# Optimization experiments

Measured on AMD Instinct MI355X. Metric: run time of the kernel, lower is better.

## Reference

```python
import jax, jax.numpy as jnp
import numpy as np

NUM_HEADS = 12
ROPE_THETA = 100.0

def _rotate_half(x):
    x1 = x[..., ::2]
    x2 = x[..., 1::2]
    return jnp.stack((-x2, x1), axis=-1).reshape(x.shape)

def _apply_rope(x, cos, sin):
    return x * cos + _rotate_half(x) * sin

def _rope_cos_sin(h, w, head_dim, theta):
    quarter = head_dim // 4  # head_dim=64 -> 16 freq bands
    inv_freq = 1.0 / theta ** (jnp.arange(quarter, dtype=jnp.float32) / max(quarter, 1))
    y = jnp.repeat(jnp.arange(h, dtype=jnp.float32), w)   # [h*w]
    xc = jnp.tile(jnp.arange(w, dtype=jnp.float32), h)    # [h*w]
    y_freqs = y[:, None] * inv_freq[None, :]               # [N, quarter]
    x_freqs = xc[:, None] * inv_freq[None, :]
    y_ang = jnp.repeat(y_freqs, 2, axis=-1)                # [N, half]
    x_ang = jnp.repeat(x_freqs, 2, axis=-1)
    ang = jnp.concatenate([y_ang, x_ang], axis=-1)         # [N, head_dim]
    return jnp.cos(ang)[None, None], jnp.sin(ang)[None, None]  # [1,1,N,hd]

def setup_inputs() -> dict:
    key = jax.random.key(0)
    ks = jax.random.split(key, 8)
    B, S, D = 8, 1025, 768
    s = 0.02
    return {
        "x": jax.random.normal(ks[0], (B, S, D), jnp.float32),
        "q_w": jax.random.normal(ks[1], (D, D), jnp.float32) * s,
        "q_b": jax.random.normal(ks[2], (D,), jnp.float32) * s,
        "k_w": jax.random.normal(ks[3], (D, D), jnp.float32) * s,
        "v_w": jax.random.normal(ks[4], (D, D), jnp.float32) * s,
        "v_b": jax.random.normal(ks[5], (D,), jnp.float32) * s,
        "o_w": jax.random.normal(ks[6], (D, D), jnp.float32) * s,
        "o_b": jax.random.normal(ks[7], (D,), jnp.float32) * s,
        "h": 32,
        "w": 32,
        "num_prefix_tokens": 1,
    }

def reference(x, q_w, q_b, k_w, v_w, v_b, o_w, o_b, h, w, num_prefix_tokens):
    B, S, D = x.shape
    H = NUM_HEADS
    hd = D // H
    scale = hd ** -0.5
    p = num_prefix_tokens

    def proj(W, b):
        y = jnp.einsum('bsd,ed->bse', x, W)
        if b is not None:
            y = y + b
        return y.reshape(B, S, H, hd).transpose(0, 2, 1, 3)  # [B,H,S,hd]

    q = proj(q_w, q_b)
    k = proj(k_w, None)
    v = proj(v_w, v_b)

    cos, sin = _rope_cos_sin(h, w, hd, ROPE_THETA)
    q = jnp.concatenate([q[:, :, :p], _apply_rope(q[:, :, p:], cos, sin)], axis=2)
    k = jnp.concatenate([k[:, :, :p], _apply_rope(k[:, :, p:], cos, sin)], axis=2)

    attn = jnp.einsum('bhqd,bhkd->bhqk', q * scale, k)
    attn = jax.nn.softmax(attn, axis=-1)
    out = jnp.einsum('bhqk,bhkd->bhqd', attn, v)
    out = out.transpose(0, 2, 1, 3).reshape(B, S, D)
    return jnp.einsum('bsd,ed->bse', out, o_w) + o_b
```

## Files before the change

### kernel.cpp

```cpp
#include <hip/hip_runtime.h>

typedef unsigned short u16;
typedef unsigned int   u32;
typedef __attribute__((ext_vector_type(4))) short s4;
typedef __attribute__((ext_vector_type(8))) short s8;
typedef __attribute__((ext_vector_type(4))) float f4;
typedef __attribute__((ext_vector_type(16))) float f16v;

#define NB   8
#define SEQ  1025
#define DIM  768
#define NH   12
#define HD   64
#define MPAD 8320
#define MV   8200
#define SQP  1040
#define SKP  1088
#define NQKV 2304
#define BHT  96
#define QSCALE 0.1803368801111204f

__device__ __forceinline__ u16 f2bf(float f) {
  u32 u = __builtin_bit_cast(u32, f);
  u += 0x7fffu + ((u >> 16) & 1u);
  return (u16)(u >> 16);
}
__device__ __forceinline__ float bf2f(u16 h) {
  return __builtin_bit_cast(float, ((u32)h) << 16);
}
__device__ __forceinline__ float exp2f_(float x) {
#if __has_builtin(__builtin_amdgcn_exp2f)
  return __builtin_amdgcn_exp2f(x);
#else
  return exp2f(x);
#endif
}
__device__ __forceinline__ u32 cvtpk(float a, float b) {
  u32 r;
  asm("v_cvt_pk_bf16_f32 %0, %1, %2" : "=v"(r) : "v"(a), "v"(b));
  return r;
}

typedef const __attribute__((address_space(1))) void cas1v;
typedef __attribute__((address_space(3))) void as3v;
__device__ __forceinline__ void gload16(const void* g, void* l) {
  __builtin_amdgcn_global_load_lds((cas1v*)g, (as3v*)l, 16, 0, 0);
}

#define MFMA16(a, b, c) __builtin_amdgcn_mfma_f32_16x16x32_bf16(a, b, c, 0, 0, 0)
#define MFMA32(a, b, c) __builtin_amdgcn_mfma_f32_32x32x16_bf16(a, b, c, 0, 0, 0)

__global__ void conv_x(const float* __restrict__ x, u16* __restrict__ xb) {
  int i = blockIdx.x * 256 + threadIdx.x;
  int e = i * 4;
  int row = e / DIM;
  s4 o;
  if (row < MV) {
    float4 v = *(const float4*)(x + e);
    o[0] = (short)f2bf(v.x); o[1] = (short)f2bf(v.y);
    o[2] = (short)f2bf(v.z); o[3] = (short)f2bf(v.w);
  } else {
    o = (s4){0, 0, 0, 0};
  }
  *(s4*)(xb + e) = o;
}

__global__ void conv_w(const float* __restrict__ qw, const float* __restrict__ kw,
                       const float* __restrict__ vw, const float* __restrict__ ow,
                       const float* __restrict__ qb, const float* __restrict__ vb,
                       u16* __restrict__ wqkv, u16* __restrict__ wo, float* __restrict__ biasq) {
  int i = blockIdx.x * 256 + threadIdx.x;
  wqkv[i]           = f2bf(qw[i]);
  wqkv[i + 589824]  = f2bf(kw[i]);
  wqkv[i + 1179648] = f2bf(vw[i]);
  wo[i]             = f2bf(ow[i]);
  if (i < NQKV) biasq[i] = (i < 768) ? qb[i] : (i < 1536 ? 0.f : vb[i - 1536]);
}

template <int MODE>
__global__ __launch_bounds__(256) void gemm_bt(const u16* __restrict__ A, const u16* __restrict__ Bm,
                                               float* __restrict__ Cf, const float* __restrict__ bias,
                                               u16* __restrict__ Ql, u16* __restrict__ Kl,
                                               u16* __restrict__ Vr,
                                               int N, int K, int Mvalid, int nnt) {
  __shared__ u16 As[2][128 * 32];
  __shared__ u16 Bs[2][128 * 32];
  int tid = threadIdx.x;
  int lane = tid & 63, wave = tid >> 6;
  int g = lane >> 4, c16 = lane & 15;
  int nwg = gridDim.x, orig = blockIdx.x;
  int qd = nwg >> 3, rm = nwg & 7, xcd = orig & 7;
  int wgid = (xcd < rm ? xcd * (qd + 1) : rm * (qd + 1) + (xcd - rm) * qd) + (orig >> 3);
  int m0 = (wgid / nnt) * 128, n0 = (wgid % nnt) * 128;
  int wm = wave >> 1, wn = wave & 1;
  f4 acc[4][4] = {};

  int ldrow = wave * 16 + (lane >> 2);
  int ldk = (lane & 3) * 8;
  const u16* Asrc = A + (size_t)(m0 + ldrow) * K + ldk;
  const u16* Bsrc = Bm + (size_t)(n0 + ldrow) * K + ldk;

  auto stage = [&](int buf, int k0) {
    u16* aw = &As[buf][wave * 512];
    u16* bw = &Bs[buf][wave * 512];
    gload16(Asrc + k0, aw);
    gload16(Asrc + 64 * K + k0, aw + 2048);
    gload16(Bsrc + k0, bw);
    gload16(Bsrc + 64 * K + k0, bw + 2048);
  };

  stage(0, 0);
  __syncthreads();
  int nk = K >> 5;
  for (int t = 0; t < nk; t++) {
    int buf = t & 1;
    if (t + 1 < nk) stage(buf ^ 1, (t + 1) << 5);
    s8 af[4], bf[4];
#pragma unroll
    for (int i = 0; i < 4; i++) {
      af[i] = *(const s8*)(&As[buf][(wm * 64 + i * 16 + c16) * 32 + g * 8]);
      bf[i] = *(const s8*)(&Bs[buf][(wn * 64 + i * 16 + c16) * 32 + g * 8]);
    }
    __builtin_amdgcn_s_setprio(1);
#pragma unroll
    for (int i = 0; i < 4; i++)
#pragma unroll
      for (int j = 0; j < 4; j++)
        acc[i][j] = MFMA16(af[i], bf[j], acc[i][j]);
    __builtin_amdgcn_s_setprio(0);
    __syncthreads();
  }

#pragma unroll
  for (int i = 0; i < 4; i++)
#pragma unroll
    for (int j = 0; j < 4; j++) {
      int n = n0 + wn * 64 + j * 16 + c16;
      float bv = bias[n];
#pragma unroll
      for (int r = 0; r < 4; r++) {
        int m = m0 + wm * 64 + i * 16 + g * 4 + r;
        if (m < Mvalid) {
          float v = acc[i][j][r] + bv;
          if (MODE == 1) {
            Cf[(size_t)m * N + n] = v;
          } else {
            int b = m / 1025, s = m - b * 1025;
            int nh6 = n >> 6, part = nh6 / 12, h = nh6 - part * 12, d = n & 63;
            u16 o = f2bf(v);
            if (part == 0)      Ql[((size_t)((b * NH + h) * SQP + s)) * HD + d] = o;
            else if (part == 1) Kl[((size_t)((b * NH + h) * SKP + s)) * HD + d] = o;
            else                Vr[(size_t)m * DIM + (n - 1536)] = o;
          }
        }
      }
    }
}

__global__ void rope_qk(u16* __restrict__ Ql, u16* __restrict__ Kl) {
  int t = blockIdx.x * 256 + threadIdx.x;
  int j = t & 31;
  int rem = t >> 5;
  int s = rem % SKP;
  int bh = rem / SKP;
  if (bh >= BHT) return;
  size_t qoff = ((size_t)(bh * SQP + s)) * HD + 2 * j;
  size_t koff = ((size_t)(bh * SKP + s)) * HD + 2 * j;
  if (s >= SEQ) {
    *(u32*)(Kl + koff) = 0;
    if (s < SQP) *(u32*)(Ql + qoff) = 0;
    return;
  }
  u32 qp = *(const u32*)(Ql + qoff);
  u32 kp = *(const u32*)(Kl + koff);
  float q0 = bf2f((u16)qp), q1 = bf2f((u16)(qp >> 16));
  float k0 = bf2f((u16)kp), k1 = bf2f((u16)(kp >> 16));
  float cs = 1.f, sn = 0.f;
  if (s > 0) {
    int tok = s - 1;
    int pos = (j < 16) ? (tok >> 5) : (tok & 31);
    int f = j & 15;
    float ang = (float)pos * __expf((float)f * -0.28782313662425572f);
    __sincosf(ang, &sn, &cs);
  }
  float q0r = q0 * cs - q1 * sn, q1r = q1 * cs + q0 * sn;
  float k0r = k0 * cs - k1 * sn, k1r = k1 * cs + k0 * sn;
  *(u32*)(Ql + qoff) = (u32)f2bf(q0r * QSCALE) | ((u32)f2bf(q1r * QSCALE) << 16);
  *(u32*)(Kl + koff) = (u32)f2bf(k0r) | ((u32)f2bf(k1r) << 16);
}

__global__ void v_trans(const u16* __restrict__ Vr, u16* __restrict__ Vt) {
  __shared__ u16 tile[32][72];
  int bh = blockIdx.x / 34, st = blockIdx.x % 34;
  int b = bh / NH, h = bh % NH;
  int s0 = st * 32;
  int tid = threadIdx.x;
  {
    int sl = tid >> 3, c8 = (tid & 7) * 8;
    int s = s0 + sl;
    s8 v = (s8){0, 0, 0, 0, 0, 0, 0, 0};
    if (s < SEQ) v = *(const s8*)(Vr + ((size_t)(b * SEQ + s)) * DIM + h * HD + c8);
    *(s8*)&tile[sl][c8] = v;
  }
  __syncthreads();
  {
    int d = tid >> 2, sc = (tid & 3) * 8;
    s8 o;
#pragma unroll
    for (int u = 0; u < 8; u++) o[u] = (short)tile[sc + u][d];
    *(s8*)(Vt + ((size_t)(bh * HD + d)) * SKP + s0 + sc) = o;
  }
}

__global__ __launch_bounds__(256) void attn_k(const u16* __restrict__ Q, const u16* __restrict__ K,
                                              const u16* __restrict__ V, u16* __restrict__ Ao) {
  __shared__ u16 lds[2][2][64 * 64];
  int bh = blockIdx.x;
  int tid = threadIdx.x;
  int wave = tid >> 6, lane = tid & 63;
  int q32 = lane & 31, h = lane >> 5;
  int b = bh / NH, hh = bh % NH;
  int qb = blockIdx.y * 128 + wave * 32;
  if (qb > SEQ - 32) qb = SEQ - 32;
  const u16* Qb = Q + (size_t)bh * SQP * HD;
  const u16* Kb = K + (size_t)bh * SKP * HD;
  const u16* Vb = V + (size_t)bh * HD * SKP;

  s8 qf[4];
#pragma unroll
  for (int t = 0; t < 4; t++)
    qf[t] = *(const s8*)(Qb + (size_t)(qb + q32) * HD + 16 * t + 8 * h);

  f16v o0 = {}, o1 = {};
  float mrun = -3e38f, lrun = 0.f;
  int swz = (q32 & 7) << 4;

  auto stage = [&](int buf, int kv0) {
#pragma unroll
    for (int i = 0; i < 2; i++) {
      int sb = i * 4096 + tid * 16;
      int row = sb >> 7;
      int ch = (sb >> 4) & 7;
      int so = (ch ^ (row & 7)) * 8;
      u16* kd = &lds[buf][0][(i * 4096 + wave * 1024) >> 1];
      u16* vd = &lds[buf][1][(i * 4096 + wave * 1024) >> 1];
      gload16(Kb + (size_t)(kv0 + row) * HD + so, kd);
      gload16(Vb + (size_t)row * SKP + kv0 + so, vd);
    }
  };

  stage(0, 0);
  __syncthreads();

  for (int c = 0; c < 17; c++) {
    int buf = c & 1;
    if (c < 16) stage(buf ^ 1, (c + 1) * 64);
    const char* Ks = (const char*)&lds[buf][0][0];
    const char* Vs = (const char*)&lds[buf][1][0];

    f16v st0 = {}, st1 = {};
    __builtin_amdgcn_s_setprio(1);
#pragma unroll
    for (int t = 0; t < 4; t++) {
      int off = (32 * t + 16 * h) ^ swz;
      s8 a0 = *(const s8*)(Ks + q32 * 128 + off);
      s8 a1 = *(const s8*)(Ks + (32 + q32) * 128 + off);
      st0 = MFMA32(a0, qf[t], st0);
      st1 = MFMA32(a1, qf[t], st1);
    }
    __builtin_amdgcn_s_setprio(0);

    if (c == 16) {
      st0[0] = h ? -3e38f : st0[0];
#pragma unroll
      for (int r = 1; r < 16; r++) st0[r] = -3e38f;
#pragma unroll
      for (int r = 0; r < 16; r++) st1[r] = -3e38f;
    }

    float pmax = -3e38f;
#pragma unroll
    for (int r = 0; r < 16; r++) pmax = fmaxf(pmax, fmaxf(st0[r], st1[r]));
    pmax = fmaxf(pmax, __shfl_xor(pmax, 32));

    if (!__all(pmax <= mrun + 11.5f)) {
      float mnew = fmaxf(mrun, pmax);
      float cf = exp2f_(mrun - mnew);
      lrun *= cf;
      mrun = mnew;
#pragma unroll
      for (int r = 0; r < 16; r++) {
        float c2 = __shfl(cf, (r & 3) + 8 * (r >> 2) + 4 * h);
        o0[r] *= c2;
        o1[r] *= c2;
      }
    }

    float ps = 0.f;
#pragma unroll
    for (int r = 0; r < 16; r++) {
      st0[r] = exp2f_(st0[r] - mrun);
      st1[r] = exp2f_(st1[r] - mrun);
      ps += st0[r] + st1[r];
    }
    ps += __shfl_xor(ps, 32);
    lrun += ps;

    __builtin_amdgcn_s_setprio(1);
#pragma unroll
    for (int s = 0; s < 4; s++) {
      union { s8 v; u32 w[4]; } pa;
#pragma unroll
      for (int i = 0; i < 4; i++) {
        float plo = (s < 2) ? st0[8 * (s & 1) + 2 * i]     : st1[8 * (s & 1) + 2 * i];
        float phi = (s < 2) ? st0[8 * (s & 1) + 2 * i + 1] : st1[8 * (s & 1) + 2 * i + 1];
        pa.w[i] = cvtpk(plo, phi);
      }
      int ob = (32 * s + 8 * h) ^ swz;
      const char* v0 = Vs + q32 * 128;
      const char* v1 = Vs + (32 + q32) * 128;
      s4 lo, hi;
      lo = *(const s4*)(v0 + ob); hi = *(const s4*)(v0 + (ob ^ 16));
      s8 vf0 = (s8){lo[0], lo[1], lo[2], lo[3], hi[0], hi[1], hi[2], hi[3]};
      lo = *(const s4*)(v1 + ob); hi = *(const s4*)(v1 + (ob ^ 16));
      s8 vf1 = (s8){lo[0], lo[1], lo[2], lo[3], hi[0], hi[1], hi[2], hi[3]};
      o0 = MFMA32(pa.v, vf0, o0);
      o1 = MFMA32(pa.v, vf1, o1);
    }
    __builtin_amdgcn_s_setprio(0);
    __syncthreads();
  }

  float rl = 1.0f / lrun;
#pragma unroll
  for (int r = 0; r < 16; r++) {
    int cr = (r & 3) + 8 * (r >> 2) + 4 * h;
    float sc = __shfl(rl, cr);
    u16* dst = Ao + (size_t)(b * SEQ + qb + cr) * DIM + hh * HD;
    dst[q32]      = f2bf(o0[r] * sc);
    dst[32 + q32] = f2bf(o1[r] * sc);
  }
}

extern "C" void kernel_launch(void* const* d_in, const int* in_sizes, int n_in,
                              void* d_out, int out_size, void* d_ws, size_t ws_size,
                              hipStream_t stream) {
  const float* x  = (const float*)d_in[0];
  const float* qw = (const float*)d_in[1];
  const float* qb = (const float*)d_in[2];
  const float* kw = (const float*)d_in[3];
  const float* vw = (const float*)d_in[4];
  const float* vb = (const float*)d_in[5];
  const float* ow = (const float*)d_in[6];
  const float* ob = (const float*)d_in[7];
  float* out = (float*)d_out;

  char* ws = (char*)d_ws;
  u16*   xb   = (u16*)(ws);
  u16*   wqkv = (u16*)(ws + 12779520);
  u16*   wo   = (u16*)(ws + 16318464);
  float* bq   = (float*)(ws + 17498112);
  u16*   Vr   = (u16*)(ws + 17507328);
  u16*   Ql   = (u16*)(ws + 30102528);
  u16*   Kl   = (u16*)(ws + 42882048);
  u16*   Vt   = (u16*)(ws + 56251392);
  u16*   Ao   = xb;

  conv_x<<<6240, 256, 0, stream>>>(x, xb);
  conv_w<<<2304, 256, 0, stream>>>(qw, kw, vw, ow, qb, vb, wqkv, wo, bq);
  gemm_bt<2><<<1170, 256, 0, stream>>>(xb, wqkv, nullptr, bq, Ql, Kl, Vr, NQKV, DIM, MV, 18);
  rope_qk<<<13056, 256, 0, stream>>>(Ql, Kl);
  v_trans<<<3264, 256, 0, stream>>>(Vr, Vt);
  attn_k<<<dim3(96, 9), 256, 0, stream>>>(Ql, Kl, Vt, Ao);
  gemm_bt<1><<<390, 256, 0, stream>>>(Ao, wo, out, ob, nullptr, nullptr, nullptr, DIM, DIM, MV, 6);
}
```

Before: 169.2 us.

## Write V in MFMA-fragment layout from QKV GEMM and drop LDS staging in attention

```diff
diff --git a/kernel.cpp b/kernel.cpp
--- a/kernel.cpp
+++ b/kernel.cpp
@@ -12,10 +12,10 @@
 #define DIM  768
 #define NH   12
 #define HD   64
-#define MPAD 8320
 #define MV   8200
 #define SQP  1040
 #define SKP  1088
+#define NG16 68
 #define NQKV 2304
 #define BHT  96
 #define QSCALE 0.1803368801111204f
@@ -81,7 +81,7 @@
 __global__ __launch_bounds__(256) void gemm_bt(const u16* __restrict__ A, const u16* __restrict__ Bm,
                                                float* __restrict__ Cf, const float* __restrict__ bias,
                                                u16* __restrict__ Ql, u16* __restrict__ Kl,
-                                               u16* __restrict__ Vr,
+                                               u16* __restrict__ Vp,
                                                int N, int K, int Mvalid, int nnt) {
   __shared__ u16 As[2][128 * 32];
   __shared__ u16 Bs[2][128 * 32];
@@ -146,11 +146,15 @@
             Cf[(size_t)m * N + n] = v;
           } else {
             int b = m / 1025, s = m - b * 1025;
-            int nh6 = n >> 6, part = nh6 / 12, h = nh6 - part * 12, d = n & 63;
+            int nh6 = n >> 6, part = nh6 / 12, hq = nh6 - part * 12, d = n & 63;
             u16 o = f2bf(v);
-            if (part == 0)      Ql[((size_t)((b * NH + h) * SQP + s)) * HD + d] = o;
-            else if (part == 1) Kl[((size_t)((b * NH + h) * SKP + s)) * HD + d] = o;
-            else                Vr[(size_t)m * DIM + (n - 1536)] = o;
+            if (part == 0)      Ql[((size_t)((b * NH + hq) * SQP + s)) * HD + d] = o;
+            else if (part == 1) Kl[((size_t)((b * NH + hq) * SKP + s)) * HD + d] = o;
+            else {
+              int g16 = s >> 4, rr = s & 15;
+              int mp = (rr & 3) | (((rr >> 3) & 1) << 2) | (((rr >> 2) & 1) << 3);
+              Vp[((size_t)((b * NH + hq) * NG16 + g16) * HD + d) * 16 + mp] = o;
+            }
           }
         }
       }
@@ -189,42 +193,17 @@
   *(u32*)(Kl + koff) = (u32)f2bf(k0r) | ((u32)f2bf(k1r) << 16);
 }
 
-__global__ void v_trans(const u16* __restrict__ Vr, u16* __restrict__ Vt) {
-  __shared__ u16 tile[32][72];
-  int bh = blockIdx.x / 34, st = blockIdx.x % 34;
-  int b = bh / NH, h = bh % NH;
-  int s0 = st * 32;
-  int tid = threadIdx.x;
-  {
-    int sl = tid >> 3, c8 = (tid & 7) * 8;
-    int s = s0 + sl;
-    s8 v = (s8){0, 0, 0, 0, 0, 0, 0, 0};
-    if (s < SEQ) v = *(const s8*)(Vr + ((size_t)(b * SEQ + s)) * DIM + h * HD + c8);
-    *(s8*)&tile[sl][c8] = v;
-  }
-  __syncthreads();
-  {
-    int d = tid >> 2, sc = (tid & 3) * 8;
-    s8 o;
-#pragma unroll
-    for (int u = 0; u < 8; u++) o[u] = (short)tile[sc + u][d];
-    *(s8*)(Vt + ((size_t)(bh * HD + d)) * SKP + s0 + sc) = o;
-  }
-}
-
 __global__ __launch_bounds__(256) void attn_k(const u16* __restrict__ Q, const u16* __restrict__ K,
-                                              const u16* __restrict__ V, u16* __restrict__ Ao) {
-  __shared__ u16 lds[2][2][64 * 64];
+                                              const u16* __restrict__ Vp, u16* __restrict__ Ao) {
   int bh = blockIdx.x;
-  int tid = threadIdx.x;
-  int wave = tid >> 6, lane = tid & 63;
+  int wave = threadIdx.x >> 6, lane = threadIdx.x & 63;
   int q32 = lane & 31, h = lane >> 5;
   int b = bh / NH, hh = bh % NH;
   int qb = blockIdx.y * 128 + wave * 32;
   if (qb > SEQ - 32) qb = SEQ - 32;
   const u16* Qb = Q + (size_t)bh * SQP * HD;
-  const u16* Kb = K + (size_t)bh * SKP * HD;
-  const u16* Vb = V + (size_t)bh * HD * SKP;
+  const u16* Kb = K + (size_t)bh * SKP * HD + q32 * HD + 8 * h;
+  const u16* Vb = Vp + (size_t)bh * NG16 * 1024 + q32 * 16 + 8 * h;
 
   s8 qf[4];
 #pragma unroll
@@ -233,42 +212,32 @@
 
   f16v o0 = {}, o1 = {};
   float mrun = -3e38f, lrun = 0.f;
-  int swz = (q32 & 7) << 4;
-
-  auto stage = [&](int buf, int kv0) {
-#pragma unroll
-    for (int i = 0; i < 2; i++) {
-      int sb = i * 4096 + tid * 16;
-      int row = sb >> 7;
-      int ch = (sb >> 4) & 7;
-      int so = (ch ^ (row & 7)) * 8;
-      u16* kd = &lds[buf][0][(i * 4096 + wave * 1024) >> 1];
-      u16* vd = &lds[buf][1][(i * 4096 + wave * 1024) >> 1];
-      gload16(Kb + (size_t)(kv0 + row) * HD + so, kd);
-      gload16(Vb + (size_t)row * SKP + kv0 + so, vd);
-    }
-  };
-
-  stage(0, 0);
-  __syncthreads();
 
   for (int c = 0; c < 17; c++) {
-    int buf = c & 1;
-    if (c < 16) stage(buf ^ 1, (c + 1) * 64);
-    const char* Ks = (const char*)&lds[buf][0][0];
-    const char* Vs = (const char*)&lds[buf][1][0];
-
+    const u16* kc = Kb + c * (64 * HD);
     f16v st0 = {}, st1 = {};
-    __builtin_amdgcn_s_setprio(1);
-#pragma unroll
-    for (int t = 0; t < 4; t++) {
-      int off = (32 * t + 16 * h) ^ swz;
-      s8 a0 = *(const s8*)(Ks + q32 * 128 + off);
-      s8 a1 = *(const s8*)(Ks + (32 + q32) * 128 + off);
-      st0 = MFMA32(a0, qf[t], st0);
-      st1 = MFMA32(a1, qf[t], st1);
-    }
-    __builtin_amdgcn_s_setprio(0);
+    {
+      s8 a0[4], a1[4];
+#pragma unroll
+      for (int t = 0; t < 4; t++) a0[t] = *(const s8*)(kc + 16 * t);
+#pragma unroll
+      for (int t = 0; t < 4; t++) a1[t] = *(const s8*)(kc + 32 * HD + 16 * t);
+      __builtin_amdgcn_s_setprio(1);
+#pragma unroll
+      for (int t = 0; t < 4; t++) {
+        st0 = MFMA32(a0[t], qf[t], st0);
+        st1 = MFMA32(a1[t], qf[t], st1);
+      }
+      __builtin_amdgcn_s_setprio(0);
+    }
+
+    const u16* vc = Vb + c * 4096;
+    s8 vf0[4], vf1[4];
+#pragma unroll
+    for (int s = 0; s < 4; s++) {
+      vf0[s] = *(const s8*)(vc + s * 1024);
+      vf1[s] = *(const s8*)(vc + s * 1024 + 512);
+    }
 
     if (c == 16) {
       st0[0] = h ? -3e38f : st0[0];
@@ -278,10 +247,15 @@
       for (int r = 0; r < 16; r++) st1[r] = -3e38f;
     }
 
-    float pmax = -3e38f;
-#pragma unroll
-    for (int r = 0; r < 16; r++) pmax = fmaxf(pmax, fmaxf(st0[r], st1[r]));
-    pmax = fmaxf(pmax, __shfl_xor(pmax, 32));
+    float mx[8];
+#pragma unroll
+    for (int r = 0; r < 8; r++)
+      mx[r] = fmaxf(fmaxf(st0[r], st0[r + 8]), fmaxf(st1[r], st1[r + 8]));
+#pragma unroll
+    for (int w = 4; w >= 1; w >>= 1)
+#pragma unroll
+      for (int r = 0; r < w; r++) mx[r] = fmaxf(mx[r], mx[r + w]);
+    float pmax = fmaxf(mx[0], __shfl_xor(mx[0], 32));
 
     if (!__all(pmax <= mrun + 11.5f)) {
       float mnew = fmaxf(mrun, pmax);
@@ -296,15 +270,19 @@
       }
     }
 
-    float ps = 0.f;
+    float sm[8];
 #pragma unroll
     for (int r = 0; r < 16; r++) {
       st0[r] = exp2f_(st0[r] - mrun);
       st1[r] = exp2f_(st1[r] - mrun);
-      ps += st0[r] + st1[r];
-    }
-    ps += __shfl_xor(ps, 32);
-    lrun += ps;
+    }
+#pragma unroll
+    for (int r = 0; r < 8; r++) sm[r] = (st0[r] + st0[r + 8]) + (st1[r] + st1[r + 8]);
+#pragma unroll
+    for (int w = 4; w >= 1; w >>= 1)
+#pragma unroll
+      for (int r = 0; r < w; r++) sm[r] += sm[r + w];
+    lrun += sm[0] + __shfl_xor(sm[0], 32);
 
     __builtin_amdgcn_s_setprio(1);
 #pragma unroll
@@ -316,19 +294,10 @@
         float phi = (s < 2) ? st0[8 * (s & 1) + 2 * i + 1] : st1[8 * (s & 1) + 2 * i + 1];
         pa.w[i] = cvtpk(plo, phi);
       }
-      int ob = (32 * s + 8 * h) ^ swz;
-      const char* v0 = Vs + q32 * 128;
-      const char* v1 = Vs + (32 + q32) * 128;
-      s4 lo, hi;
-      lo = *(const s4*)(v0 + ob); hi = *(const s4*)(v0 + (ob ^ 16));
-      s8 vf0 = (s8){lo[0], lo[1], lo[2], lo[3], hi[0], hi[1], hi[2], hi[3]};
-      lo = *(const s4*)(v1 + ob); hi = *(const s4*)(v1 + (ob ^ 16));
-      s8 vf1 = (s8){lo[0], lo[1], lo[2], lo[3], hi[0], hi[1], hi[2], hi[3]};
-      o0 = MFMA32(pa.v, vf0, o0);
-      o1 = MFMA32(pa.v, vf1, o1);
+      o0 = MFMA32(pa.v, vf0[s], o0);
+      o1 = MFMA32(pa.v, vf1[s], o1);
     }
     __builtin_amdgcn_s_setprio(0);
-    __syncthreads();
   }
 
   float rl = 1.0f / lrun;
@@ -360,17 +329,16 @@
   u16*   wqkv = (u16*)(ws + 12779520);
   u16*   wo   = (u16*)(ws + 16318464);
   float* bq   = (float*)(ws + 17498112);
-  u16*   Vr   = (u16*)(ws + 17507328);
-  u16*   Ql   = (u16*)(ws + 30102528);
-  u16*   Kl   = (u16*)(ws + 42882048);
-  u16*   Vt   = (u16*)(ws + 56251392);
+  u16*   Ql   = (u16*)(ws + 17507328);
+  u16*   Kl   = (u16*)(ws + 30286848);
+  u16*   Vp   = (u16*)(ws + 43656192);
   u16*   Ao   = xb;
 
   conv_x<<<6240, 256, 0, stream>>>(x, xb);
   conv_w<<<2304, 256, 0, stream>>>(qw, kw, vw, ow, qb, vb, wqkv, wo, bq);
-  gemm_bt<2><<<1170, 256, 0, stream>>>(xb, wqkv, nullptr, bq, Ql, Kl, Vr, NQKV, DIM, MV, 18);
+  hipMemsetAsync(Vp, 0, 13369344, stream);
+  gemm_bt<2><<<1170, 256, 0, stream>>>(xb, wqkv, nullptr, bq, Ql, Kl, Vp, NQKV, DIM, MV, 18);
   rope_qk<<<13056, 256, 0, stream>>>(Ql, Kl);
-  v_trans<<<3264, 256, 0, stream>>>(Vr, Vt);
-  attn_k<<<dim3(96, 9), 256, 0, stream>>>(Ql, Kl, Vt, Ao);
+  attn_k<<<dim3(96, 9), 256, 0, stream>>>(Ql, Kl, Vp, Ao);
   gemm_bt<1><<<390, 256, 0, stream>>>(Ao, wo, out, ob, nullptr, nullptr, nullptr, DIM, DIM, MV, 6);
 }
```

After: 202.1 us. 1.19x slower.
